# Optimization experiments

Measured on AMD Instinct MI355X. Metric: run time of the kernel, lower is better.

## Reference

```python
import jax, jax.numpy as jnp
import numpy as np

DIM = 1024
NUM_HEADS = 16
HEAD_DIM = DIM // NUM_HEADS
SCALE = HEAD_DIM ** -0.5


def setup_inputs() -> dict:
    key = jax.random.key(0)
    k1, k2, k3 = jax.random.split(key, 3)
    x = jax.random.normal(k1, (2, 2048, DIM), dtype=jnp.float32)
    # nn.Linear weights: stored as [out, in]; y = x @ W.T
    w_qkv = jax.random.normal(k2, (3 * DIM, DIM), dtype=jnp.float32) * (DIM ** -0.5)
    w_proj = jax.random.normal(k3, (DIM, DIM), dtype=jnp.float32) * (DIM ** -0.5)
    return {"x": x, "w_qkv": w_qkv, "w_proj": w_proj}


def reference(x, w_qkv, w_proj):
    B, L, D = x.shape
    qkv = jnp.einsum("bld,ed->ble", x, w_qkv)  # [B, L, 3*D]
    qkv = qkv.reshape(B, L, 3, NUM_HEADS, HEAD_DIM).transpose(2, 0, 3, 1, 4)
    q, k, v = qkv[0], qkv[1], qkv[2]  # each [B, H, L, hd]
    attn = jnp.einsum("bhqd,bhkd->bhqk", q, k) * SCALE
    attn = jax.nn.softmax(attn, axis=-1)
    out = jnp.einsum("bhqk,bhkd->bhqd", attn, v)  # [B, H, L, hd]
    out = out.transpose(0, 2, 1, 3).reshape(B, L, D)
    return jnp.einsum("bld,ed->ble", out, w_proj)
```

## Files before the change

kernel.cpp:

```cpp
#include <hip/hip_runtime.h>
#include <math.h>
#include <stdint.h>

#define B_ 2
#define L_ 2048
#define D_ 1024
#define H_ 16
#define HD_ 64
#define QSCALE_ 0.1803368801f

typedef __attribute__((ext_vector_type(8))) short short8;
typedef __attribute__((ext_vector_type(4))) short short4v;
typedef __attribute__((ext_vector_type(4))) float float4v;

#if defined(__has_builtin)
#if __has_builtin(__builtin_amdgcn_exp2f)
#define EXP2F(x) __builtin_amdgcn_exp2f(x)
#endif
#endif
#ifndef EXP2F
#define EXP2F(x) exp2f(x)
#endif

__device__ __forceinline__ short f2bf(float f) {
    union { float f; unsigned u; } x; x.f = f;
    unsigned r = x.u + 0x7fffu + ((x.u >> 16) & 1u);
    return (short)(r >> 16);
}

__device__ __forceinline__ unsigned fbits(float f) {
    union { float f; unsigned u; } x; x.f = f;
    return x.u;
}

__device__ __forceinline__ unsigned pk_bf_trunc(float a, float b) {
    return __builtin_amdgcn_perm(fbits(b), fbits(a), 0x07060302u);
}

__global__ __launch_bounds__(256) void cvt_all(const float* __restrict__ x,
                                               const float* __restrict__ wqkv,
                                               const float* __restrict__ wproj,
                                               short* __restrict__ xb,
                                               short* __restrict__ wqkvb,
                                               short* __restrict__ wprojb) {
    int i = blockIdx.x * 256 + threadIdx.x;
    const float* in;
    short* out;
    int idx;
    if (i < 1048576)      { in = x;     out = xb;     idx = i; }
    else if (i < 1835008) { in = wqkv;  out = wqkvb;  idx = i - 1048576; }
    else                  { in = wproj; out = wprojb; idx = i - 1835008; }
    float4 v = ((const float4*)in)[idx];
    short4v o;
    o.x = f2bf(v.x); o.y = f2bf(v.y); o.z = f2bf(v.z); o.w = f2bf(v.w);
    ((short4v*)out)[idx] = o;
}

#define LDA_ 40
__global__ __launch_bounds__(512) void gemm_qkv_bf16(const short* __restrict__ A,
                                                     const short* __restrict__ Bm,
                                                     short* __restrict__ Qb,
                                                     short* __restrict__ Kb,
                                                     short* __restrict__ Vb) {
    __shared__ short smem[20480];
    const int tid = threadIdx.x;
    const int w = tid >> 6, l = tid & 63;
    const int lm = l & 15, q = l >> 4;
    const int bid = blockIdx.x;
    const int xcd = bid & 7;
    const int grp = bid >> 3;
    const int n_tile = xcd + 8 * (grp % 3);
    const int m_tile = grp / 3;
    const int m0 = m_tile * 128, n0 = n_tile * 128;
    const int wm = w >> 2, wn = w & 3;

    const int srow = tid >> 2;
    const int sc8  = (tid & 3) * 8;
    const int soff = srow * LDA_ + sc8;
    const short* Ag = A  + (size_t)(m0 + srow) * 1024 + sc8;
    const short* Bg = Bm + (size_t)(n0 + srow) * 1024 + sc8;

    float4v acc[4][2];
#pragma unroll
    for (int mt = 0; mt < 4; ++mt)
#pragma unroll
        for (int nt = 0; nt < 2; ++nt) acc[mt][nt] = (float4v){0.f, 0.f, 0.f, 0.f};

    {
        short8 a0 = *(const short8*)(Ag);
        short8 b0 = *(const short8*)(Bg);
        *(short8*)(smem + soff) = a0;
        *(short8*)(smem + 10240 + soff) = b0;
    }
    short8 ar = *(const short8*)(Ag + 32);
    short8 br = *(const short8*)(Bg + 32);

    for (int t = 0; t < 32; ++t) {
        const int cur = t & 1;
        short* Asc = smem + cur * 5120;
        short* Asn = smem + (1 - cur) * 5120;
        short* Bsc = smem + 10240 + cur * 5120;
        short* Bsn = smem + 10240 + (1 - cur) * 5120;

        __syncthreads();

        if (t < 31) {
            *(short8*)(Asn + soff) = ar;
            *(short8*)(Bsn + soff) = br;
        }
        if (t < 30) {
            const int k0 = (t + 2) * 32;
            ar = *(const short8*)(Ag + k0);
            br = *(const short8*)(Bg + k0);
        }

        short8 af[4], bfr[2];
#pragma unroll
        for (int mt = 0; mt < 4; ++mt)
            af[mt] = *(const short8*)(Asc + (wm * 64 + mt * 16 + lm) * LDA_ + q * 8);
#pragma unroll
        for (int nt = 0; nt < 2; ++nt)
            bfr[nt] = *(const short8*)(Bsc + (wn * 32 + nt * 16 + lm) * LDA_ + q * 8);
#pragma unroll
        for (int mt = 0; mt < 4; ++mt)
#pragma unroll
            for (int nt = 0; nt < 2; ++nt)
                acc[mt][nt] = __builtin_amdgcn_mfma_f32_16x16x32_bf16(af[mt], bfr[nt], acc[mt][nt], 0, 0, 0);
    }

    const int which = n0 >> 10;
    if (which < 2) {
        short* dst = (which == 0) ? Qb : Kb;
        const float sc = (which == 0) ? QSCALE_ : 1.0f;
#pragma unroll
        for (int half = 0; half < 2; ++half) {
            __syncthreads();
            if (wm == half) {
#pragma unroll
                for (int mt = 0; mt < 4; ++mt)
#pragma unroll
                    for (int nt = 0; nt < 2; ++nt)
#pragma unroll
                        for (int r = 0; r < 4; ++r)
                            smem[(mt * 16 + q * 4 + r) * 128 + wn * 32 + nt * 16 + lm] =
                                f2bf(acc[mt][nt][r] * sc);
            }
            __syncthreads();
#pragma unroll
            for (int j = 0; j < 2; ++j) {
                const int x = tid + 512 * j;
                const int row = x >> 4, c = x & 15;
                short8 v = *(const short8*)(smem + row * 128 + c * 8);
                const int m = m0 + half * 64 + row;
                const int b = m >> 11, ll = m & 2047;
                const int n = n0 + c * 8;
                const int hh = (n & 1023) >> 6, d = n & 63;
                *(short8*)(dst + (((size_t)b * H_ + hh) * L_ + ll) * HD_ + d) = v;
            }
        }
    } else {
        const int mbase = m0 + wm * 64;
        const int b = mbase >> 11;
        const int llb = (mbase & 2047);
#pragma unroll
        for (int mt = 0; mt < 4; ++mt) {
            const int ll = llb + (mt >> 1) * 32 + q * 8 + (mt & 1) * 4;
#pragma unroll
            for (int nt = 0; nt < 2; ++nt) {
                const int n = n0 + wn * 32 + nt * 16 + lm;
                const int h = (n & 1023) >> 6, d = n & 63;
                short4v pk;
                pk.x = f2bf(acc[mt][nt][0]); pk.y = f2bf(acc[mt][nt][1]);
                pk.z = f2bf(acc[mt][nt][2]); pk.w = f2bf(acc[mt][nt][3]);
                *(short4v*)(Vb + (((size_t)b * H_ + h) * HD_ + d) * L_ + ll) = pk;
            }
        }
    }
}

__global__ __launch_bounds__(512) void attn_mfma(const short* __restrict__ Qb,
                                                 const short* __restrict__ Kb,
                                                 const short* __restrict__ Vtg,
                                                 short* __restrict__ Ob) {
    __shared__ short KV[4 * 4096];

    const int tid = threadIdx.x;
    const int w = tid >> 6, l = tid & 63;
    const int lm = l & 15, q = l >> 4;
    const int bid = blockIdx.x;
    const int grp = bid >> 3;
    const int bh = (bid & 7) * 4 + (grp & 3);
    const int qt = grp >> 2;

    const short* Qg = Qb  + ((size_t)bh * L_ + qt * 128) * HD_;
    const short* Kg = Kb  + (size_t)bh * L_ * HD_;
    const short* Vg = Vtg + (size_t)bh * HD_ * L_;

    short* Qs = KV + 8192;
#pragma unroll
    for (int t = 0; t < 2; ++t) {
        int idx = tid + 512 * t;
        int row = idx >> 3, c = idx & 7;
        short8 v = *(const short8*)(Qg + row * 64 + c * 8);
        *(short8*)(Qs + row * 64 + ((c ^ (row & 7)) * 8)) = v;
    }

    const int srow = tid >> 3;
    const int sc   = tid & 7;
    const int koff = srow * 64 + ((sc ^ (srow & 7)) * 8);

    {
        short8 ka = *(const short8*)(Kg + (size_t)srow * 64 + sc * 8);
        short8 va = *(const short8*)(Vg + (size_t)srow * L_ + sc * 8);
        *(short8*)(KV + koff) = ka;
        *(short8*)(KV + 4096 + koff) = va;
    }
    short8 kra = *(const short8*)(Kg + (size_t)(64 + srow) * 64 + sc * 8);
    short8 vra = *(const short8*)(Vg + (size_t)srow * L_ + 64 + sc * 8);

    __syncthreads();

    short8 qf[2];
#pragma unroll
    for (int kh = 0; kh < 2; ++kh) {
        int row = w * 16 + lm;
        int ch = kh * 4 + q;
        qf[kh] = *(const short8*)(Qs + row * 64 + ((ch ^ (row & 7)) * 8));
    }

    int offA0[4], offA1[4], offV[2][4];
#pragma unroll
    for (int nt = 0; nt < 4; ++nt) {
        const int arow = nt * 16 + lm;
        offA0[nt] = arow * 64 + ((q ^ (arow & 7)) * 8);
        offA1[nt] = arow * 64 + (((4 + q) ^ (arow & 7)) * 8);
#pragma unroll
        for (int kh = 0; kh < 2; ++kh)
            offV[kh][nt] = arow * 64 + (((kh * 4 + q) ^ (arow & 7)) * 8);
    }

    float4v o[4];
#pragma unroll
    for (int mt = 0; mt < 4; ++mt) o[mt] = (float4v){0.f, 0.f, 0.f, 0.f};
    float lsum = 0.f;

#pragma unroll 2
    for (int t = 0; t < 32; ++t) {
        const int cur = t & 1;
        short* Kl = KV + cur * 8192;
        short* Vt = Kl + 4096;
        short* Kn = KV + (1 - cur) * 8192;
        short* Vn = Kn + 4096;

        __syncthreads();

        if (t < 31) {
            *(short8*)(Kn + koff) = kra;
            *(short8*)(Vn + koff) = vra;
        }
        if (t < 30) {
            kra = *(const short8*)(Kg + (size_t)((t + 2) * 64 + srow) * 64 + sc * 8);
            vra = *(const short8*)(Vg + (size_t)srow * L_ + (t + 2) * 64 + sc * 8);
        }

        float4v st[4];
#pragma unroll
        for (int nt = 0; nt < 4; ++nt) {
            short8 a0 = *(const short8*)(Kl + offA0[nt]);
            short8 a1 = *(const short8*)(Kl + offA1[nt]);
            float4v z = (float4v){0.f, 0.f, 0.f, 0.f};
            z = __builtin_amdgcn_mfma_f32_16x16x32_bf16(a0, qf[0], z, 0, 0, 0);
            z = __builtin_amdgcn_mfma_f32_16x16x32_bf16(a1, qf[1], z, 0, 0, 0);
            st[nt] = z;
        }

        float e[4][4];
#pragma unroll
        for (int nt = 0; nt < 4; ++nt) {
            e[nt][0] = EXP2F(st[nt][0]);
            e[nt][1] = EXP2F(st[nt][1]);
            e[nt][2] = EXP2F(st[nt][2]);
            e[nt][3] = EXP2F(st[nt][3]);
            lsum += (e[nt][0] + e[nt][1]) + (e[nt][2] + e[nt][3]);
        }
        short8 pb[2];
        {
            union { short8 s8; unsigned u[4]; } p0, p1;
            p0.u[0] = pk_bf_trunc(e[0][0], e[0][1]);
            p0.u[1] = pk_bf_trunc(e[0][2], e[0][3]);
            p0.u[2] = pk_bf_trunc(e[1][0], e[1][1]);
            p0.u[3] = pk_bf_trunc(e[1][2], e[1][3]);
            p1.u[0] = pk_bf_trunc(e[2][0], e[2][1]);
            p1.u[1] = pk_bf_trunc(e[2][2], e[2][3]);
            p1.u[2] = pk_bf_trunc(e[3][0], e[3][1]);
            p1.u[3] = pk_bf_trunc(e[3][2], e[3][3]);
            pb[0] = p0.s8;
            pb[1] = p1.s8;
        }

#pragma unroll
        for (int kh = 0; kh < 2; ++kh)
#pragma unroll
            for (int mt = 0; mt < 4; ++mt) {
                short8 va = *(const short8*)(Vt + offV[kh][mt]);
                o[mt] = __builtin_amdgcn_mfma_f32_16x16x32_bf16(va, pb[kh], o[mt], 0, 0, 0);
            }
    }

    float s = lsum;
    s += __shfl_xor(s, 16);
    s += __shfl_xor(s, 32);
    const float inv = 1.f / s;
    short* OgBase = Ob + ((size_t)bh * L_ + qt * 128) * HD_;
    const int qrow = w * 16 + lm;
#pragma unroll
    for (int mt = 0; mt < 4; ++mt) {
        short4v pk;
        pk.x = f2bf(o[mt][0] * inv);
        pk.y = f2bf(o[mt][1] * inv);
        pk.z = f2bf(o[mt][2] * inv);
        pk.w = f2bf(o[mt][3] * inv);
        *(short4v*)(OgBase + (size_t)qrow * 64 + mt * 16 + q * 4) = pk;
    }
}

__global__ __launch_bounds__(256) void gemm_proj_bf16(const short* __restrict__ Ob,
                                                      const short* __restrict__ Wp,
                                                      float* __restrict__ out) {
    __shared__ short As[2 * 2560];
    __shared__ short Bs[2 * 5120];
    const int tid = threadIdx.x;
    const int w = tid >> 6, l = tid & 63;
    const int lm = l & 15, q = l >> 4;
    const int bid = blockIdx.x;
    const int m0 = (bid >> 3) * 64, n0 = (bid & 7) * 128;
    const int wm = w & 1, wn = w >> 1;
    const int b = m0 >> 11, l0 = m0 & 2047;

    const int srow = tid >> 2;
    const int sc8  = (tid & 3) * 8;
    const int aoff = srow * LDA_ + sc8;
    const int boff0 = aoff;
    const int boff1 = aoff + 64 * LDA_;
    const short* Agb = Ob + (((size_t)b * H_) * L_ + l0 + srow) * HD_;
    const short* Bg  = Wp + (size_t)(n0 + srow) * 1024 + sc8;

    float4v acc[2][4];
#pragma unroll
    for (int mt = 0; mt < 2; ++mt)
#pragma unroll
        for (int nt = 0; nt < 4; ++nt) acc[mt][nt] = (float4v){0.f, 0.f, 0.f, 0.f};

    {
        short8 a0 = *(const short8*)(Agb + sc8);
        short8 b0 = *(const short8*)(Bg);
        short8 b1 = *(const short8*)(Bg + 64 * 1024);
        *(short8*)(As + aoff) = a0;
        *(short8*)(Bs + boff0) = b0;
        *(short8*)(Bs + boff1) = b1;
    }
    short8 arx = *(const short8*)(Agb + 32 + sc8);
    short8 brx0 = *(const short8*)(Bg + 32);
    short8 brx1 = *(const short8*)(Bg + 64 * 1024 + 32);

    for (int t = 0; t < 32; ++t) {
        const int cur = t & 1;
        short* Asc = As + cur * 2560;
        short* Asn = As + (1 - cur) * 2560;
        short* Bsc = Bs + cur * 5120;
        short* Bsn = Bs + (1 - cur) * 5120;

        __syncthreads();

        if (t < 31) {
            *(short8*)(Asn + aoff) = arx;
            *(short8*)(Bsn + boff0) = brx0;
            *(short8*)(Bsn + boff1) = brx1;
        }
        if (t < 30) {
            const int tn = t + 2;
            const int hh = tn >> 1, d = (tn & 1) * 32 + sc8;
            arx  = *(const short8*)(Agb + (size_t)hh * L_ * HD_ + d);
            brx0 = *(const short8*)(Bg + tn * 32);
            brx1 = *(const short8*)(Bg + 64 * 1024 + tn * 32);
        }

        short8 af[2], bfr[4];
#pragma unroll
        for (int mt = 0; mt < 2; ++mt)
            af[mt] = *(const short8*)(Asc + (wm * 32 + mt * 16 + lm) * LDA_ + q * 8);
#pragma unroll
        for (int nt = 0; nt < 4; ++nt)
            bfr[nt] = *(const short8*)(Bsc + (wn * 64 + nt * 16 + lm) * LDA_ + q * 8);
#pragma unroll
        for (int mt = 0; mt < 2; ++mt)
#pragma unroll
            for (int nt = 0; nt < 4; ++nt)
                acc[mt][nt] = __builtin_amdgcn_mfma_f32_16x16x32_bf16(af[mt], bfr[nt], acc[mt][nt], 0, 0, 0);
    }

#pragma unroll
    for (int mt = 0; mt < 2; ++mt)
#pragma unroll
        for (int nt = 0; nt < 4; ++nt)
#pragma unroll
            for (int r = 0; r < 4; ++r) {
                const int m = m0 + wm * 32 + mt * 16 + q * 4 + r;
                const int n = n0 + wn * 64 + nt * 16 + lm;
                out[(size_t)m * 1024 + n] = acc[mt][nt][r];
            }
}

extern "C" void kernel_launch(void* const* d_in, const int* in_sizes, int n_in,
                              void* d_out, int out_size, void* d_ws, size_t ws_size,
                              hipStream_t stream) {
    (void)in_sizes; (void)n_in; (void)out_size; (void)ws_size;
    const float* x      = (const float*)d_in[0];
    const float* w_qkv  = (const float*)d_in[1];
    const float* w_proj = (const float*)d_in[2];

    char* ws = (char*)d_ws;
    short* xb     = (short*)(ws);
    short* wqkvb  = (short*)(ws + (8u  << 20));
    short* wprojb = (short*)(ws + (14u << 20));
    short* Qb     = (short*)(ws + (16u << 20));
    short* Kb     = (short*)(ws + (24u << 20));
    short* Vb     = (short*)(ws + (32u << 20));
    short* Ob     = (short*)(ws + (40u << 20));

    cvt_all<<<8192, 256, 0, stream>>>(x, w_qkv, w_proj, xb, wqkvb, wprojb);
    gemm_qkv_bf16 <<<768, 512, 0, stream>>>(xb, wqkvb, Qb, Kb, Vb);
    attn_mfma     <<<512, 512, 0, stream>>>(Qb, Kb, Vb, Ob);
    gemm_proj_bf16<<<512, 256, 0, stream>>>(Ob, wprojb, (float*)d_out);
}
```

Before: 181.3 us.

## Split attention KV range in halves with 256-row Q tiles and combine pass

```diff
diff --git a/kernel.cpp b/kernel.cpp
--- a/kernel.cpp
+++ b/kernel.cpp
@@ -26,6 +26,12 @@
     union { float f; unsigned u; } x; x.f = f;
     unsigned r = x.u + 0x7fffu + ((x.u >> 16) & 1u);
     return (short)(r >> 16);
+}
+
+__device__ __forceinline__ float bf2f(short s) {
+    union { unsigned u; float f; } x;
+    x.u = ((unsigned)(unsigned short)s) << 16;
+    return x.f;
 }
 
 __device__ __forceinline__ unsigned fbits(float f) {
@@ -181,29 +187,33 @@
 __global__ __launch_bounds__(512) void attn_mfma(const short* __restrict__ Qb,
                                                  const short* __restrict__ Kb,
                                                  const short* __restrict__ Vtg,
-                                                 short* __restrict__ Ob) {
+                                                 short* __restrict__ Op0,
+                                                 short* __restrict__ Op1,
+                                                 float* __restrict__ Lp0,
+                                                 float* __restrict__ Lp1) {
     __shared__ short KV[4 * 4096];
 
     const int tid = threadIdx.x;
     const int w = tid >> 6, l = tid & 63;
     const int lm = l & 15, q = l >> 4;
     const int bid = blockIdx.x;
+    const int xcd = bid & 7;
     const int grp = bid >> 3;
-    const int bh = (bid & 7) * 4 + (grp & 3);
-    const int qt = grp >> 2;
-
-    const short* Qg = Qb  + ((size_t)bh * L_ + qt * 128) * HD_;
-    const short* Kg = Kb  + (size_t)bh * L_ * HD_;
-    const short* Vg = Vtg + (size_t)bh * HD_ * L_;
-
-    short* Qs = KV + 8192;
-#pragma unroll
-    for (int t = 0; t < 2; ++t) {
-        int idx = tid + 512 * t;
-        int row = idx >> 3, c = idx & 7;
-        short8 v = *(const short8*)(Qg + row * 64 + c * 8);
-        *(short8*)(Qs + row * 64 + ((c ^ (row & 7)) * 8)) = v;
-    }
+    const int combo = xcd * 8 + (grp >> 3);
+    const int bh = combo >> 1;
+    const int half = combo & 1;
+    const int qt = grp & 7;
+
+    const short* Qg = Qb  + ((size_t)bh * L_ + qt * 256) * HD_;
+    const short* Kg = Kb  + ((size_t)bh * L_ + half * 1024) * HD_;
+    const short* Vg = Vtg + (size_t)bh * HD_ * L_ + half * 1024;
+
+    short8 qf[2][2];
+#pragma unroll
+    for (int nq = 0; nq < 2; ++nq)
+#pragma unroll
+        for (int kh = 0; kh < 2; ++kh)
+            qf[nq][kh] = *(const short8*)(Qg + (size_t)(w * 32 + nq * 16 + lm) * HD_ + (kh * 4 + q) * 8);
 
     const int srow = tid >> 3;
     const int sc   = tid & 7;
@@ -220,14 +230,6 @@
 
     __syncthreads();
 
-    short8 qf[2];
-#pragma unroll
-    for (int kh = 0; kh < 2; ++kh) {
-        int row = w * 16 + lm;
-        int ch = kh * 4 + q;
-        qf[kh] = *(const short8*)(Qs + row * 64 + ((ch ^ (row & 7)) * 8));
-    }
-
     int offA0[4], offA1[4], offV[2][4];
 #pragma unroll
     for (int nt = 0; nt < 4; ++nt) {
@@ -239,13 +241,15 @@
             offV[kh][nt] = arow * 64 + (((kh * 4 + q) ^ (arow & 7)) * 8);
     }
 
-    float4v o[4];
-#pragma unroll
-    for (int mt = 0; mt < 4; ++mt) o[mt] = (float4v){0.f, 0.f, 0.f, 0.f};
-    float lsum = 0.f;
+    float4v o[4][2];
+#pragma unroll
+    for (int mt = 0; mt < 4; ++mt)
+#pragma unroll
+        for (int nq = 0; nq < 2; ++nq) o[mt][nq] = (float4v){0.f, 0.f, 0.f, 0.f};
+    float lsum[2] = {0.f, 0.f};
 
 #pragma unroll 2
-    for (int t = 0; t < 32; ++t) {
+    for (int t = 0; t < 16; ++t) {
         const int cur = t & 1;
         short* Kl = KV + cur * 8192;
         short* Vt = Kl + 4096;
@@ -254,37 +258,41 @@
 
         __syncthreads();
 
-        if (t < 31) {
+        if (t < 15) {
             *(short8*)(Kn + koff) = kra;
             *(short8*)(Vn + koff) = vra;
         }
-        if (t < 30) {
+        if (t < 14) {
             kra = *(const short8*)(Kg + (size_t)((t + 2) * 64 + srow) * 64 + sc * 8);
             vra = *(const short8*)(Vg + (size_t)srow * L_ + (t + 2) * 64 + sc * 8);
         }
 
-        float4v st[4];
+        float4v st[4][2];
 #pragma unroll
         for (int nt = 0; nt < 4; ++nt) {
             short8 a0 = *(const short8*)(Kl + offA0[nt]);
             short8 a1 = *(const short8*)(Kl + offA1[nt]);
-            float4v z = (float4v){0.f, 0.f, 0.f, 0.f};
-            z = __builtin_amdgcn_mfma_f32_16x16x32_bf16(a0, qf[0], z, 0, 0, 0);
-            z = __builtin_amdgcn_mfma_f32_16x16x32_bf16(a1, qf[1], z, 0, 0, 0);
-            st[nt] = z;
-        }
-
-        float e[4][4];
-#pragma unroll
-        for (int nt = 0; nt < 4; ++nt) {
-            e[nt][0] = EXP2F(st[nt][0]);
-            e[nt][1] = EXP2F(st[nt][1]);
-            e[nt][2] = EXP2F(st[nt][2]);
-            e[nt][3] = EXP2F(st[nt][3]);
-            lsum += (e[nt][0] + e[nt][1]) + (e[nt][2] + e[nt][3]);
-        }
-        short8 pb[2];
-        {
+#pragma unroll
+            for (int nq = 0; nq < 2; ++nq) {
+                float4v z = (float4v){0.f, 0.f, 0.f, 0.f};
+                z = __builtin_amdgcn_mfma_f32_16x16x32_bf16(a0, qf[nq][0], z, 0, 0, 0);
+                z = __builtin_amdgcn_mfma_f32_16x16x32_bf16(a1, qf[nq][1], z, 0, 0, 0);
+                st[nt][nq] = z;
+            }
+        }
+
+        short8 pb[2][2];
+#pragma unroll
+        for (int nq = 0; nq < 2; ++nq) {
+            float e[4][4];
+#pragma unroll
+            for (int nt = 0; nt < 4; ++nt) {
+                e[nt][0] = EXP2F(st[nt][nq][0]);
+                e[nt][1] = EXP2F(st[nt][nq][1]);
+                e[nt][2] = EXP2F(st[nt][nq][2]);
+                e[nt][3] = EXP2F(st[nt][nq][3]);
+                lsum[nq] += (e[nt][0] + e[nt][1]) + (e[nt][2] + e[nt][3]);
+            }
             union { short8 s8; unsigned u[4]; } p0, p1;
             p0.u[0] = pk_bf_trunc(e[0][0], e[0][1]);
             p0.u[1] = pk_bf_trunc(e[0][2], e[0][3]);
@@ -294,8 +302,8 @@
             p1.u[1] = pk_bf_trunc(e[2][2], e[2][3]);
             p1.u[2] = pk_bf_trunc(e[3][0], e[3][1]);
             p1.u[3] = pk_bf_trunc(e[3][2], e[3][3]);
-            pb[0] = p0.s8;
-            pb[1] = p1.s8;
+            pb[0][nq] = p0.s8;
+            pb[1][nq] = p1.s8;
         }
 
 #pragma unroll
@@ -303,25 +311,57 @@
 #pragma unroll
             for (int mt = 0; mt < 4; ++mt) {
                 short8 va = *(const short8*)(Vt + offV[kh][mt]);
-                o[mt] = __builtin_amdgcn_mfma_f32_16x16x32_bf16(va, pb[kh], o[mt], 0, 0, 0);
-            }
-    }
-
-    float s = lsum;
-    s += __shfl_xor(s, 16);
-    s += __shfl_xor(s, 32);
-    const float inv = 1.f / s;
-    short* OgBase = Ob + ((size_t)bh * L_ + qt * 128) * HD_;
-    const int qrow = w * 16 + lm;
-#pragma unroll
-    for (int mt = 0; mt < 4; ++mt) {
-        short4v pk;
-        pk.x = f2bf(o[mt][0] * inv);
-        pk.y = f2bf(o[mt][1] * inv);
-        pk.z = f2bf(o[mt][2] * inv);
-        pk.w = f2bf(o[mt][3] * inv);
-        *(short4v*)(OgBase + (size_t)qrow * 64 + mt * 16 + q * 4) = pk;
-    }
+#pragma unroll
+                for (int nq = 0; nq < 2; ++nq)
+                    o[mt][nq] = __builtin_amdgcn_mfma_f32_16x16x32_bf16(va, pb[kh][nq], o[mt][nq], 0, 0, 0);
+            }
+    }
+
+#pragma unroll
+    for (int nq = 0; nq < 2; ++nq) {
+        float s = lsum[nq];
+        s += __shfl_xor(s, 16);
+        s += __shfl_xor(s, 32);
+        lsum[nq] = s;
+    }
+    short* Op = half ? Op1 : Op0;
+    float* Lp = half ? Lp1 : Lp0;
+    short* OgBase = Op + ((size_t)bh * L_ + qt * 256) * HD_;
+#pragma unroll
+    for (int nq = 0; nq < 2; ++nq) {
+        const int qrow = w * 32 + nq * 16 + lm;
+#pragma unroll
+        for (int mt = 0; mt < 4; ++mt) {
+            short4v pk;
+            pk.x = f2bf(o[mt][nq][0]);
+            pk.y = f2bf(o[mt][nq][1]);
+            pk.z = f2bf(o[mt][nq][2]);
+            pk.w = f2bf(o[mt][nq][3]);
+            *(short4v*)(OgBase + (size_t)qrow * 64 + mt * 16 + q * 4) = pk;
+        }
+    }
+    if (l < 16) {
+        const size_t rbase = (size_t)bh * L_ + qt * 256 + w * 32 + l;
+        Lp[rbase]      = lsum[0];
+        Lp[rbase + 16] = lsum[1];
+    }
+}
+
+__global__ __launch_bounds__(256) void combine_o(const short* __restrict__ Op0,
+                                                 short* __restrict__ Op1,
+                                                 const float* __restrict__ Lp0,
+                                                 const float* __restrict__ Lp1) {
+    const int i = blockIdx.x * 256 + threadIdx.x;
+    const int rg = i >> 3, cg = i & 7;
+    const float inv = 1.f / (Lp0[rg] + Lp1[rg]);
+    const size_t off = (size_t)rg * 64 + cg * 8;
+    short8 a = *(const short8*)(Op0 + off);
+    short8 b = *(const short8*)(Op1 + off);
+    short8 r;
+#pragma unroll
+    for (int j = 0; j < 8; ++j)
+        r[j] = f2bf((bf2f(a[j]) + bf2f(b[j])) * inv);
+    *(short8*)(Op1 + off) = r;
 }
 
 __global__ __launch_bounds__(256) void gemm_proj_bf16(const short* __restrict__ Ob,
@@ -428,8 +468,14 @@
     short* Vb     = (short*)(ws + (32u << 20));
     short* Ob     = (short*)(ws + (40u << 20));
 
+    short* Op0 = xb;
+    short* Op1 = Ob;
+    float* Lp0 = (float*)(ws + (8u << 20));
+    float* Lp1 = (float*)(ws + (8u << 20) + (256u << 10));
+
     cvt_all<<<8192, 256, 0, stream>>>(x, w_qkv, w_proj, xb, wqkvb, wprojb);
     gemm_qkv_bf16 <<<768, 512, 0, stream>>>(xb, wqkvb, Qb, Kb, Vb);
-    attn_mfma     <<<512, 512, 0, stream>>>(Qb, Kb, Vb, Ob);
+    attn_mfma     <<<512, 512, 0, stream>>>(Qb, Kb, Vb, Op0, Op1, Lp0, Lp1);
+    combine_o     <<<2048, 256, 0, stream>>>(Op0, Op1, Lp0, Lp1);
     gemm_proj_bf16<<<512, 256, 0, stream>>>(Ob, wprojb, (float*)d_out);
 }
```

New measurement: 179.7 us. Within noise of the previous version (-0.9%).
